# Optimization experiments

Measured on AMD Instinct MI355X. Metric: run time of the kernel, lower is better.

Reference implementation:

```python
import jax, jax.numpy as jnp
import numpy as np

B, N, K = 8, 2048, 16   # batch, points, neighbors (after dropping self)
EPS = 1e-5


def _bn(y, g, b, m, v):
    # eval-mode batchnorm over channel dim 1, y: [B,C,...]
    sh = (1, -1) + (1,) * (y.ndim - 2)
    inv = g.reshape(sh) / jnp.sqrt(v.reshape(sh) + EPS)
    return (y - m.reshape(sh)) * inv + b.reshape(sh)


def setup_inputs() -> dict:
    key = jax.random.key(0)
    ks = jax.random.split(key, 16)
    d = {}
    d["x"] = jax.random.normal(ks[0], (B, 3, N), dtype=jnp.float32)
    # pre: Conv1d(3->24, k=1) + BN
    d["w_pre"] = jax.random.normal(ks[1], (24, 3), dtype=jnp.float32) * 0.3
    d["b_pre"] = jax.random.normal(ks[2], (24,), dtype=jnp.float32) * 0.1
    d["g_pre"] = 1.0 + 0.1 * jax.random.normal(ks[3], (24,), dtype=jnp.float32)
    d["be_pre"] = 0.1 * jax.random.normal(ks[4], (24,), dtype=jnp.float32)
    d["m_pre"] = 0.1 * jax.random.normal(ks[5], (24,), dtype=jnp.float32)
    d["v_pre"] = jax.random.uniform(ks[6], (24,), minval=0.5, maxval=1.5, dtype=jnp.float32)
    # shared_mlp_1: Conv2d(48->12, 1, bias=False) + BN
    d["w1"] = jax.random.normal(ks[7], (12, 48), dtype=jnp.float32) * 0.15
    d["g1"] = 1.0 + 0.1 * jax.random.normal(ks[8], (12,), dtype=jnp.float32)
    d["be1"] = 0.1 * jax.random.normal(ks[9], (12,), dtype=jnp.float32)
    d["m1"] = 0.1 * jax.random.normal(ks[10], (12,), dtype=jnp.float32)
    d["v1"] = jax.random.uniform(ks[11], (12,), minval=0.5, maxval=1.5, dtype=jnp.float32)
    # shared_mlp_2: Conv2d(60->12, 1, bias=False) + BN
    d["w2"] = jax.random.normal(ks[12], (12, 60), dtype=jnp.float32) * 0.15
    d["g2"] = 1.0 + 0.1 * jax.random.normal(ks[13], (12,), dtype=jnp.float32)
    d["be2"] = 0.1 * jax.random.normal(ks[14], (12,), dtype=jnp.float32)
    d["m2"] = 0.1 * jax.random.normal(ks[15], (12,), dtype=jnp.float32)
    d["v2"] = jnp.ones((12,), dtype=jnp.float32)
    # shared_mlp_3: Conv2d(72->12, 1, bias=False), no BN
    d["w3"] = jax.random.normal(jax.random.fold_in(key, 99), (12, 72), dtype=jnp.float32) * 0.15
    return d


def reference(x, w_pre, b_pre, g_pre, be_pre, m_pre, v_pre,
              w1, g1, be1, m1, v1, w2, g2, be2, m2, v2, w3):
    # pre: 1x1 conv1d + BN + ReLU -> [B,24,N]
    pre = jnp.einsum('oc,bcn->bon', w_pre, x) + b_pre[None, :, None]
    pre = jax.nn.relu(_bn(pre, g_pre, be_pre, m_pre, v_pre))

    # kNN on xyz = x.detach(): [B,N,3]
    pts = jax.lax.stop_gradient(jnp.swapaxes(x, 1, 2))
    sq = jnp.sum(pts * pts, axis=-1)                              # [B,N]
    d2 = sq[:, :, None] + sq[:, None, :] - 2.0 * jnp.einsum('bnc,bmc->bnm', pts, pts)
    _, idx = jax.lax.top_k(-d2, K + 1)                             # nearest K+1 incl. self
    idx = idx[..., 1:]                                             # drop self -> [B,N,K]

    # gather neighbor features: [B,24,N,K]
    grouped = jax.vmap(lambda f, i: f[:, i])(pre, idx)
    center = jnp.broadcast_to(pre[..., None], grouped.shape)
    y = jnp.concatenate([center, grouped], axis=1)                 # [B,48,N,K]

    h1 = jax.nn.relu(_bn(jnp.einsum('oc,bcnk->bonk', w1, y), g1, be1, m1, v1))
    y = jnp.concatenate([h1, y], axis=1)                           # [B,60,N,K]
    h2 = jax.nn.relu(_bn(jnp.einsum('oc,bcnk->bonk', w2, y), g2, be2, m2, v2))
    y = jnp.concatenate([h2, y], axis=1)                           # [B,72,N,K]
    h3 = jnp.einsum('oc,bcnk->bonk', w3, y)
    y = jnp.concatenate([h3, y], axis=1)                           # [B,84,N,K]

    y = jnp.max(y, axis=-1)                                        # maxpool over neighbors -> [B,84,N]
    return jnp.concatenate([y, x], axis=1)                         # [B,87,N]
```

## Files before the change

### kernel.cpp

```cpp
#include <hip/hip_runtime.h>
#include <math.h>

#define EPS 1e-5f
#define NBATCH 8
#define NPTS 2048
#define KNB 16
#define BIG 3.2e38f

#define CHUNK_PTS 32
#define KNN_BLKS (NBATCH * 64)
#define THREADS 512
#define FUSED_LDS 49152

#define WS_PRE 0
#define WS_AUX (16384 * 24)
#define WS_IDX (WS_AUX + 16384 * 72)

__device__ __forceinline__ float dist2f(float mex, float mey, float mez,
                                        float sqn, float4 q) {
  float dot2 = fmaf(mex, q.x, fmaf(mey, q.y, __fmul_rn(mez, q.z)));
  return __fsub_rn(__fadd_rn(sqn, q.w), dot2);
}

template <bool HASSELF>
__device__ __forceinline__ void scan_slice(const float4* __restrict__ Cs, int selfc,
                                           float mex, float mey, float mez,
                                           float sqn, float L[16]) {
  for (int c0 = 0; c0 < 128; c0 += 16) {
    float S[16];
#pragma unroll
    for (int cc = 0; cc < 16; ++cc) {
      float4 q = Cs[c0 + cc];
      float d2 = dist2f(mex, mey, mez, sqn, q);
      if (HASSELF) S[cc] = ((c0 + cc) == selfc) ? BIG : d2;
      else         S[cc] = d2;
    }
#pragma unroll
    for (int pw = 1; pw < 16; pw <<= 1) {
#pragma unroll
      for (int k = pw; k >= 1; k >>= 1) {
#pragma unroll
        for (int j = (k & (pw - 1)); j + k < 16; j += 2 * k) {
#pragma unroll
          for (int i = 0; i < k; ++i) {
            int a = i + j, bq = i + j + k;
            if (bq < 16 && (a / (2 * pw) == bq / (2 * pw))) {
              float lo = fminf(S[a], S[bq]);
              float hi = fmaxf(S[a], S[bq]);
              S[a] = lo; S[bq] = hi;
            }
          }
        }
      }
    }
    float m[16];
#pragma unroll
    for (int i = 0; i < 16; ++i) m[i] = fminf(L[i], S[15 - i]);
#pragma unroll
    for (int d = 8; d >= 1; d >>= 1) {
#pragma unroll
      for (int i = 0; i < 16; ++i) {
        if (!(i & d)) {
          float lo = fminf(m[i], m[i | d]);
          float hi = fmaxf(m[i], m[i | d]);
          m[i] = lo; m[i | d] = hi;
        }
      }
    }
#pragma unroll
    for (int i = 0; i < 16; ++i) L[i] = m[i];
  }
}

__global__ __launch_bounds__(THREADS, 6) void fused_kernel(
    const float* __restrict__ x,
    const float* __restrict__ w_pre, const float* __restrict__ b_pre,
    const float* __restrict__ g_pre, const float* __restrict__ be_pre,
    const float* __restrict__ m_pre, const float* __restrict__ v_pre,
    const float* __restrict__ w1, const float* __restrict__ g1,
    const float* __restrict__ be1, const float* __restrict__ m1,
    const float* __restrict__ v1,
    const float* __restrict__ w2, const float* __restrict__ g2,
    const float* __restrict__ be2, const float* __restrict__ m2,
    const float* __restrict__ v2, const float* __restrict__ w3,
    float* __restrict__ pre, float* __restrict__ aux,
    int* __restrict__ knn_out) {
  extern __shared__ char smem[];
  float4* C4   = (float4*)smem;
  float* slist = (float*)(smem + 32768);
  float* fwp   = slist;
  float* fbp   = fwp + 72;
  float* fw1t  = fbp + 24;
  float* fb1   = fw1t + 576;
  float* fw2t  = fb1 + 12;
  float* fb2   = fw2t + 720;
  float* fw3t  = fb2 + 12;
  float* sinv1 = fw3t + 576;
  float* sinv2 = sinv1 + 12;
  float* sinvP = sinv2 + 12;
  float* sd2  = slist;
  int*   sidx = (int*)(slist + 640);
  int*   scnt = (int*)(slist + 1280);

  int tid = threadIdx.x;
  int bi = blockIdx.x;
  int b = bi >> 6, chunk = bi & 63;
  const float* xb = x + (size_t)b * 3 * NPTS;

  for (int j = tid; j < NPTS; j += THREADS) {
    float xx = xb[j], yy = xb[NPTS + j], zz = xb[2 * NPTS + j];
    float sq = __fadd_rn(__fadd_rn(__fmul_rn(xx, xx), __fmul_rn(yy, yy)),
                         __fmul_rn(zz, zz));
    C4[j] = make_float4(2.0f * xx, 2.0f * yy, 2.0f * zz, sq);
  }
  if (tid < 24) sinvP[tid] = g_pre[tid] / sqrtf(v_pre[tid] + EPS);
  if (tid < 12) { sinv1[tid] = g1[tid] / sqrtf(v1[tid] + EPS);
                  sinv2[tid] = g2[tid] / sqrtf(v2[tid] + EPS); }
  __syncthreads();
  if (tid < 72) fwp[tid] = w_pre[tid] * sinvP[tid / 3];
  if (tid < 24) fbp[tid] = (b_pre[tid] - m_pre[tid]) * sinvP[tid] + be_pre[tid];
  if (tid < 12) { fb1[tid] = be1[tid] - m1[tid] * sinv1[tid];
                  fb2[tid] = be2[tid] - m2[tid] * sinv2[tid]; }
  for (int j = tid; j < 576; j += THREADS) { int i = j / 12, o = j - i * 12; fw1t[j] = w1[o * 48 + i] * sinv1[o]; }
  for (int j = tid; j < 720; j += THREADS) { int i = j / 12, o = j - i * 12; fw2t[j] = w2[o * 60 + i] * sinv2[o]; }
  for (int j = tid; j < 576; j += THREADS) { int i = j / 12, o = j - i * 12; fw3t[j] = w3[o * 72 + 24 + i]; }
  __syncthreads();

  {
    int r = tid & 15, pt = tid >> 4;
    int n0 = chunk * CHUNK_PTS + pt;
    size_t pgl = (size_t)(b << 11) + n0;
    float x0 = xb[n0], x1 = xb[NPTS + n0], x2 = xb[2 * NPTS + n0];
    float pr[24];
#pragma unroll
    for (int c = 0; c < 24; ++c) {
      float v = fmaf(fwp[c * 3 + 0], x0,
                fmaf(fwp[c * 3 + 1], x1,
                fmaf(fwp[c * 3 + 2], x2, fbp[c])));
      pr[c] = fmaxf(v, 0.f);
    }
    if (r == 12) {
      float4* o4 = (float4*)(pre + pgl * 24);
#pragma unroll
      for (int i = 0; i < 6; ++i)
        o4[i] = make_float4(pr[4*i], pr[4*i+1], pr[4*i+2], pr[4*i+3]);
    }
    if (r < 12) {
      int o = r;
      float u1 = fb1[o], a1 = 0.f, u2 = fb2[o], a2 = 0.f, u3 = 0.f, a3 = 0.f;
#pragma unroll
      for (int i = 0; i < 24; ++i) {
        u1 = fmaf(fw1t[i * 12 + o],        pr[i], u1);
        a1 = fmaf(fw1t[(24 + i) * 12 + o], pr[i], a1);
        u2 = fmaf(fw2t[(12 + i) * 12 + o], pr[i], u2);
        a2 = fmaf(fw2t[(36 + i) * 12 + o], pr[i], a2);
        u3 = fmaf(fw3t[i * 12 + o],        pr[i], u3);
        a3 = fmaf(fw3t[(24 + i) * 12 + o], pr[i], a3);
      }
      float* A = aux + pgl * 72;
      A[o] = u1; A[12 + o] = u2; A[24 + o] = u3;
      A[36 + o] = a1; A[48 + o] = a2; A[60 + o] = a3;
    }
  }
  __syncthreads();

  int p = tid & 31, s = tid >> 5;
  int w = tid >> 6;
  int n = chunk * CHUNK_PTS + p;
  float4 me4 = C4[n];
  float mex = 0.5f * me4.x, mey = 0.5f * me4.y, mez = 0.5f * me4.z;
  float sqn = me4.w;
  const float4* Cs = C4 + s * 128;
  int selfc = n - s * 128;
  int wself = chunk >> 3;
  float L[16];
#pragma unroll
  for (int t = 0; t < 16; ++t) L[t] = BIG;
  if (w == wself) scan_slice<true >(Cs, selfc, mex, mey, mez, sqn, L);
  else            scan_slice<false>(Cs, selfc, mex, mey, mez, sqn, L);
  {
    float bb[16], m16[16];
#pragma unroll
    for (int i = 0; i < 16; ++i) bb[i] = __shfl_xor(L[i], 32, 64);
#pragma unroll
    for (int i = 0; i < 16; ++i) m16[i] = fminf(L[i], bb[15 - i]);
#pragma unroll
    for (int d = 8; d >= 1; d >>= 1) {
#pragma unroll
      for (int i = 0; i < 16; ++i) {
        if (!(i & d)) {
          float lo = fminf(m16[i], m16[i | d]);
          float hi = fmaxf(m16[i], m16[i | d]);
          m16[i] = lo; m16[i | d] = hi;
        }
      }
    }
    if (!(s & 1)) {
#pragma unroll
      for (int i = 0; i < 16; ++i) slist[(w * 16 + i) * 32 + p] = m16[i];
    }
  }
  __syncthreads();
  for (int W = 4; W >= 1; W >>= 1) {
    int u = tid >> 5;
    bool act = (u < W);
    float a[16], bb[16];
    if (act) {
#pragma unroll
      for (int i = 0; i < 16; ++i) a[i]  = slist[((2 * u) * 16 + i) * 32 + p];
#pragma unroll
      for (int i = 0; i < 16; ++i) bb[i] = slist[((2 * u + 1) * 16 + i) * 32 + p];
    }
    __syncthreads();
    if (act) {
      float m16[16];
#pragma unroll
      for (int i = 0; i < 16; ++i) m16[i] = fminf(a[i], bb[15 - i]);
#pragma unroll
      for (int d = 8; d >= 1; d >>= 1) {
#pragma unroll
        for (int i = 0; i < 16; ++i) {
          if (!(i & d)) {
            float lo = fminf(m16[i], m16[i | d]);
            float hi = fmaxf(m16[i], m16[i | d]);
            m16[i] = lo; m16[i | d] = hi;
          }
        }
      }
#pragma unroll
      for (int i = 0; i < 16; ++i) slist[(u * 16 + i) * 32 + p] = m16[i];
    }
    __syncthreads();
  }
  float tau = slist[15 * 32 + p];
  __syncthreads();
  for (int j = tid; j < 32 * 20; j += THREADS) sidx[j] = 0;
  if (tid < 32) scnt[tid] = 0;
  __syncthreads();
  if (w == wself) {
#pragma unroll 4
    for (int c = 0; c < 128; ++c) {
      float4 q = Cs[c];
      float d2 = dist2f(mex, mey, mez, sqn, q);
      int j = s * 128 + c;
      if (d2 <= tau && j != n) {
        int pos = atomicAdd(&scnt[p], 1);
        if (pos < 20) { sd2[p * 20 + pos] = d2; sidx[p * 20 + pos] = j; }
      }
    }
  } else {
#pragma unroll 4
    for (int c = 0; c < 128; ++c) {
      float4 q = Cs[c];
      float d2 = dist2f(mex, mey, mez, sqn, q);
      int j = s * 128 + c;
      if (d2 <= tau) {
        int pos = atomicAdd(&scnt[p], 1);
        if (pos < 20) { sd2[p * 20 + pos] = d2; sidx[p * 20 + pos] = j; }
      }
    }
  }
  __syncthreads();
  if (tid < 32) {
    int c = scnt[tid]; if (c > 20) c = 20;
    if (c > 16) {
      for (int t = 0; t < 16; ++t) {
        int best = t;
        for (int u = t + 1; u < c; ++u) {
          float da = sd2[tid * 20 + u], db = sd2[tid * 20 + best];
          int ia = sidx[tid * 20 + u], ib = sidx[tid * 20 + best];
          if (da < db || (da == db && ia < ib)) best = u;
        }
        float td = sd2[tid * 20 + t]; sd2[tid * 20 + t] = sd2[tid * 20 + best]; sd2[tid * 20 + best] = td;
        int ti = sidx[tid * 20 + t]; sidx[tid * 20 + t] = sidx[tid * 20 + best]; sidx[tid * 20 + best] = ti;
      }
    }
  }
  __syncthreads();
  {
    int pp = tid >> 4, kk = tid & 15;
    knn_out[((size_t)b * NPTS + chunk * CHUNK_PTS + pp) * KNB + kk] = sidx[pp * 20 + kk];
  }
}

__global__ __launch_bounds__(256) void mlp_kernel(
    const float* __restrict__ pre, const float* __restrict__ aux,
    const int* __restrict__ knn, const float* __restrict__ x,
    const float* __restrict__ w2, const float* __restrict__ g2,
    const float* __restrict__ v2, const float* __restrict__ w3,
    float* __restrict__ out) {
  __shared__ float sW2h[144], sW3h2[144], sW3h1[144];
  __shared__ float sout[87 * 16];
  int tid = threadIdx.x;
  if (tid < 144) {
    int o = tid / 12, i = tid - o * 12;
    float inv2 = g2[o] / sqrtf(v2[o] + EPS);
    sW2h[tid]  = w2[o * 60 + i] * inv2;
    sW3h2[tid] = w3[o * 72 + i];
    sW3h1[tid] = w3[o * 72 + 12 + i];
  }
  __syncthreads();
  int k = tid & 15, pl = tid >> 4;
  int p = blockIdx.x * 16 + pl;
  int b = p >> 11, n = p & (NPTS - 1);
  int nb = knn[(size_t)p * KNB + k];
  const float4* u4 = (const float4*)(aux + (size_t)p * 72);
  const float4* a4 = (const float4*)(aux + ((size_t)(b << 11) + nb) * 72 + 36);
  float uc[36], av[36];
#pragma unroll
  for (int i = 0; i < 9; ++i) {
    float4 t = u4[i];
    uc[4*i] = t.x; uc[4*i+1] = t.y; uc[4*i+2] = t.z; uc[4*i+3] = t.w;
    float4 t2 = a4[i];
    av[4*i] = t2.x; av[4*i+1] = t2.y; av[4*i+2] = t2.z; av[4*i+3] = t2.w;
  }
  float h1[12], h2[12], h3[12];
#pragma unroll
  for (int o = 0; o < 12; ++o) h1[o] = fmaxf(uc[o] + av[o], 0.f);
#pragma unroll
  for (int o = 0; o < 12; ++o) {
    float a = uc[12 + o] + av[12 + o];
#pragma unroll
    for (int i = 0; i < 12; ++i) a = fmaf(sW2h[o * 12 + i], h1[i], a);
    h2[o] = fmaxf(a, 0.f);
  }
#pragma unroll
  for (int o = 0; o < 12; ++o) {
    float a = uc[24 + o] + av[24 + o];
#pragma unroll
    for (int i = 0; i < 12; ++i) a = fmaf(sW3h2[o * 12 + i], h2[i], a);
#pragma unroll
    for (int i = 0; i < 12; ++i) a = fmaf(sW3h1[o * 12 + i], h1[i], a);
    h3[o] = a;
  }
  float nbf[24];
  const float4* pn4 = (const float4*)(pre + ((size_t)(b << 11) + nb) * 24);
#pragma unroll
  for (int i = 0; i < 6; ++i) {
    float4 t = pn4[i];
    nbf[4*i] = t.x; nbf[4*i+1] = t.y; nbf[4*i+2] = t.z; nbf[4*i+3] = t.w;
  }
#pragma unroll
  for (int m = 1; m < 16; m <<= 1) {
#pragma unroll
    for (int o = 0; o < 12; ++o) {
      h1[o] = fmaxf(h1[o], __shfl_xor(h1[o], m, 16));
      h2[o] = fmaxf(h2[o], __shfl_xor(h2[o], m, 16));
      h3[o] = fmaxf(h3[o], __shfl_xor(h3[o], m, 16));
    }
#pragma unroll
    for (int i = 0; i < 24; ++i)
      nbf[i] = fmaxf(nbf[i], __shfl_xor(nbf[i], m, 16));
  }
  if (k == 0) {
    const float4* c4 = (const float4*)(pre + (size_t)p * 24);
#pragma unroll
    for (int o = 0; o < 12; ++o) {
      sout[(0  + o) * 16 + pl] = h3[o];
      sout[(12 + o) * 16 + pl] = h2[o];
      sout[(24 + o) * 16 + pl] = h1[o];
    }
#pragma unroll
    for (int i = 0; i < 6; ++i) {
      float4 t = c4[i];
      sout[(36 + 4*i    ) * 16 + pl] = t.x;
      sout[(36 + 4*i + 1) * 16 + pl] = t.y;
      sout[(36 + 4*i + 2) * 16 + pl] = t.z;
      sout[(36 + 4*i + 3) * 16 + pl] = t.w;
    }
#pragma unroll
    for (int i = 0; i < 24; ++i) sout[(60 + i) * 16 + pl] = nbf[i];
    const float* xb = x + (size_t)b * 3 * NPTS + n;
    sout[84 * 16 + pl] = xb[0];
    sout[85 * 16 + pl] = xb[NPTS];
    sout[86 * 16 + pl] = xb[2 * NPTS];
  }
  __syncthreads();
  int n0 = (blockIdx.x * 16) & (NPTS - 1);
  float* ob = out + (size_t)b * 87 * NPTS;
  for (int j2 = tid; j2 < 87 * 16; j2 += 256) {
    int c = j2 >> 4, i = j2 & 15;
    ob[(size_t)c * NPTS + n0 + i] = sout[j2];
  }
}

extern "C" void kernel_launch(void* const* d_in, const int* in_sizes, int n_in,
                              void* d_out, int out_size, void* d_ws, size_t ws_size,
                              hipStream_t stream) {
  (void)in_sizes; (void)n_in; (void)out_size; (void)ws_size;
  const float* x     = (const float*)d_in[0];
  const float* w_pre = (const float*)d_in[1];
  const float* b_pre = (const float*)d_in[2];
  const float* g_pre = (const float*)d_in[3];
  const float* be_pre= (const float*)d_in[4];
  const float* m_pre = (const float*)d_in[5];
  const float* v_pre = (const float*)d_in[6];
  const float* w1    = (const float*)d_in[7];
  const float* g1    = (const float*)d_in[8];
  const float* be1   = (const float*)d_in[9];
  const float* m1    = (const float*)d_in[10];
  const float* v1    = (const float*)d_in[11];
  const float* w2    = (const float*)d_in[12];
  const float* g2    = (const float*)d_in[13];
  const float* be2   = (const float*)d_in[14];
  const float* m2    = (const float*)d_in[15];
  const float* v2    = (const float*)d_in[16];
  const float* w3    = (const float*)d_in[17];
  float* ws  = (float*)d_ws;
  float* pre = ws + WS_PRE;
  float* aux = ws + WS_AUX;
  int*   knn = (int*)(ws + WS_IDX);
  float* out = (float*)d_out;

  fused_kernel<<<KNN_BLKS, THREADS, FUSED_LDS, stream>>>(
      x, w_pre, b_pre, g_pre, be_pre, m_pre, v_pre,
      w1, g1, be1, m1, v1, w2, g2, be2, m2, v2, w3,
      pre, aux, knn);
  mlp_kernel<<<NBATCH * NPTS / 16, 256, 0, stream>>>(pre, aux, knn, x,
                                                     w2, g2, v2, w3, out);
}
```

Before: 151.5 us.

## Precompute point coordinate table in separate kernel and fold distance into FMAs

Adds a prep kernel that builds a per-batch float4 table of negated doubled coordinates and squared norms once in global memory, so each fused block copies it into LDS instead of recomputing it from strided x reads. The distance formula is rewritten as a single FMA chain using the negated coordinates, which saves an instruction per candidate. The second candidate-collection pass now reads coordinates from the global table (likely L2-cached) instead of LDS. The extra kernel launch and the global reads in that pass add cost, and the fused FMA can change rounding, which may alter neighbor ties.

```diff
diff --git a/kernel.cpp b/kernel.cpp
--- a/kernel.cpp
+++ b/kernel.cpp
@@ -15,11 +15,11 @@
 #define WS_PRE 0
 #define WS_AUX (16384 * 24)
 #define WS_IDX (WS_AUX + 16384 * 72)
+#define WS_C4G (WS_IDX + 16384 * 16)
 
 __device__ __forceinline__ float dist2f(float mex, float mey, float mez,
                                         float sqn, float4 q) {
-  float dot2 = fmaf(mex, q.x, fmaf(mey, q.y, __fmul_rn(mez, q.z)));
-  return __fsub_rn(__fadd_rn(sqn, q.w), dot2);
+  return fmaf(mex, q.x, fmaf(mey, q.y, fmaf(mez, q.z, __fadd_rn(sqn, q.w))));
 }
 
 template <bool HASSELF>
@@ -70,6 +70,17 @@
 #pragma unroll
     for (int i = 0; i < 16; ++i) L[i] = m[i];
   }
+}
+
+__global__ __launch_bounds__(256) void prep_kernel(
+    const float* __restrict__ x, float4* __restrict__ c4g) {
+  int i = blockIdx.x * 256 + threadIdx.x;
+  int b = i >> 11, n = i & (NPTS - 1);
+  const float* xb = x + (size_t)b * 3 * NPTS;
+  float xx = xb[n], yy = xb[NPTS + n], zz = xb[2 * NPTS + n];
+  float sq = __fadd_rn(__fadd_rn(__fmul_rn(xx, xx), __fmul_rn(yy, yy)),
+                       __fmul_rn(zz, zz));
+  c4g[i] = make_float4(-2.0f * xx, -2.0f * yy, -2.0f * zz, sq);
 }
 
 __global__ __launch_bounds__(THREADS, 6) void fused_kernel(
@@ -83,6 +94,7 @@
     const float* __restrict__ w2, const float* __restrict__ g2,
     const float* __restrict__ be2, const float* __restrict__ m2,
     const float* __restrict__ v2, const float* __restrict__ w3,
+    const float4* __restrict__ c4g,
     float* __restrict__ pre, float* __restrict__ aux,
     int* __restrict__ knn_out) {
   extern __shared__ char smem[];
@@ -105,14 +117,10 @@
   int tid = threadIdx.x;
   int bi = blockIdx.x;
   int b = bi >> 6, chunk = bi & 63;
+  int bq = b << 11;
   const float* xb = x + (size_t)b * 3 * NPTS;
 
-  for (int j = tid; j < NPTS; j += THREADS) {
-    float xx = xb[j], yy = xb[NPTS + j], zz = xb[2 * NPTS + j];
-    float sq = __fadd_rn(__fadd_rn(__fmul_rn(xx, xx), __fmul_rn(yy, yy)),
-                         __fmul_rn(zz, zz));
-    C4[j] = make_float4(2.0f * xx, 2.0f * yy, 2.0f * zz, sq);
-  }
+  for (int j = tid; j < NPTS; j += THREADS) C4[j] = c4g[bq + j];
   if (tid < 24) sinvP[tid] = g_pre[tid] / sqrtf(v_pre[tid] + EPS);
   if (tid < 12) { sinv1[tid] = g1[tid] / sqrtf(v1[tid] + EPS);
                   sinv2[tid] = g2[tid] / sqrtf(v2[tid] + EPS); }
@@ -129,7 +137,7 @@
   {
     int r = tid & 15, pt = tid >> 4;
     int n0 = chunk * CHUNK_PTS + pt;
-    size_t pgl = (size_t)(b << 11) + n0;
+    size_t pgl = (size_t)bq + n0;
     float x0 = xb[n0], x1 = xb[NPTS + n0], x2 = xb[2 * NPTS + n0];
     float pr[24];
 #pragma unroll
@@ -168,7 +176,7 @@
   int w = tid >> 6;
   int n = chunk * CHUNK_PTS + p;
   float4 me4 = C4[n];
-  float mex = 0.5f * me4.x, mey = 0.5f * me4.y, mez = 0.5f * me4.z;
+  float mex = -0.5f * me4.x, mey = -0.5f * me4.y, mez = -0.5f * me4.z;
   float sqn = me4.w;
   const float4* Cs = C4 + s * 128;
   int selfc = n - s * 128;
@@ -237,26 +245,29 @@
   for (int j = tid; j < 32 * 20; j += THREADS) sidx[j] = 0;
   if (tid < 32) scnt[tid] = 0;
   __syncthreads();
-  if (w == wself) {
+  {
+    const float4* Cg = c4g + bq + s * 128;
+    if (w == wself) {
 #pragma unroll 4
-    for (int c = 0; c < 128; ++c) {
-      float4 q = Cs[c];
-      float d2 = dist2f(mex, mey, mez, sqn, q);
-      int j = s * 128 + c;
-      if (d2 <= tau && j != n) {
-        int pos = atomicAdd(&scnt[p], 1);
-        if (pos < 20) { sd2[p * 20 + pos] = d2; sidx[p * 20 + pos] = j; }
-      }
-    }
-  } else {
+      for (int c = 0; c < 128; ++c) {
+        float4 q = Cg[c];
+        float d2 = dist2f(mex, mey, mez, sqn, q);
+        int j = s * 128 + c;
+        if (d2 <= tau && j != n) {
+          int pos = atomicAdd(&scnt[p], 1);
+          if (pos < 20) { sd2[p * 20 + pos] = d2; sidx[p * 20 + pos] = j; }
+        }
+      }
+    } else {
 #pragma unroll 4
-    for (int c = 0; c < 128; ++c) {
-      float4 q = Cs[c];
-      float d2 = dist2f(mex, mey, mez, sqn, q);
-      int j = s * 128 + c;
-      if (d2 <= tau) {
-        int pos = atomicAdd(&scnt[p], 1);
-        if (pos < 20) { sd2[p * 20 + pos] = d2; sidx[p * 20 + pos] = j; }
+      for (int c = 0; c < 128; ++c) {
+        float4 q = Cg[c];
+        float d2 = dist2f(mex, mey, mez, sqn, q);
+        int j = s * 128 + c;
+        if (d2 <= tau) {
+          int pos = atomicAdd(&scnt[p], 1);
+          if (pos < 20) { sd2[p * 20 + pos] = d2; sidx[p * 20 + pos] = j; }
+        }
       }
     }
   }
@@ -410,12 +421,14 @@
   float* pre = ws + WS_PRE;
   float* aux = ws + WS_AUX;
   int*   knn = (int*)(ws + WS_IDX);
+  float4* c4g = (float4*)(ws + WS_C4G);
   float* out = (float*)d_out;
 
+  prep_kernel<<<NBATCH * NPTS / 256, 256, 0, stream>>>(x, c4g);
   fused_kernel<<<KNN_BLKS, THREADS, FUSED_LDS, stream>>>(
       x, w_pre, b_pre, g_pre, be_pre, m_pre, v_pre,
       w1, g1, be1, m1, v1, w2, g2, be2, m2, v2, w3,
-      pre, aux, knn);
+      c4g, pre, aux, knn);
   mlp_kernel<<<NBATCH * NPTS / 16, 256, 0, stream>>>(pre, aux, knn, x,
                                                      w2, g2, v2, w3, out);
 }
```

New measurement: 160.3 us. 1.06x slower.

## Software-pipeline KNN distance batches and move candidate buffers to separate LDS

Applied to the files above, without the earlier changes.

Restructures the KNN slice scan into a fully unrolled, double-buffered sequence: the next 16 distances are loaded and computed while the previous batch is sorted and merged, aiming to hide LDS latency behind the sorting network. The candidate buffers (sd2/sidx/scnt) get their own LDS region so they can be zeroed at kernel start, which removes two barriers before the refinement pass. The distance calculation folds the -2 factor into the stored coordinates so it becomes one fma chain with no separate subtraction. In exchange, LDS per block and register pressure rise, and launch_bounds min-blocks is lowered from 6 to 4, which may reduce occupancy and changes float rounding of the distances slightly.

```diff
diff --git a/kernel.cpp b/kernel.cpp
--- a/kernel.cpp
+++ b/kernel.cpp
@@ -10,7 +10,7 @@
 #define CHUNK_PTS 32
 #define KNN_BLKS (NBATCH * 64)
 #define THREADS 512
-#define FUSED_LDS 49152
+#define FUSED_LDS 54400
 
 #define WS_PRE 0
 #define WS_AUX (16384 * 24)
@@ -18,61 +18,90 @@
 
 __device__ __forceinline__ float dist2f(float mex, float mey, float mez,
                                         float sqn, float4 q) {
-  float dot2 = fmaf(mex, q.x, fmaf(mey, q.y, __fmul_rn(mez, q.z)));
-  return __fsub_rn(__fadd_rn(sqn, q.w), dot2);
+  return fmaf(mex, q.x, fmaf(mey, q.y, fmaf(mez, q.z, __fadd_rn(sqn, q.w))));
+}
+
+__device__ __forceinline__ void sort16(float S[16]) {
+#pragma unroll
+  for (int pw = 1; pw < 16; pw <<= 1) {
+#pragma unroll
+    for (int k = pw; k >= 1; k >>= 1) {
+#pragma unroll
+      for (int j = (k & (pw - 1)); j + k < 16; j += 2 * k) {
+#pragma unroll
+        for (int i = 0; i < k; ++i) {
+          int a = i + j, bq = i + j + k;
+          if (bq < 16 && (a / (2 * pw) == bq / (2 * pw))) {
+            float lo = fminf(S[a], S[bq]);
+            float hi = fmaxf(S[a], S[bq]);
+            S[a] = lo; S[bq] = hi;
+          }
+        }
+      }
+    }
+  }
+}
+
+__device__ __forceinline__ void clean16(float m[16]) {
+#pragma unroll
+  for (int d = 8; d >= 1; d >>= 1) {
+#pragma unroll
+    for (int i = 0; i < 16; ++i) {
+      if (!(i & d)) {
+        float lo = fminf(m[i], m[i | d]);
+        float hi = fmaxf(m[i], m[i | d]);
+        m[i] = lo; m[i | d] = hi;
+      }
+    }
+  }
+}
+
+__device__ __forceinline__ void merge16(float L[16], const float S[16]) {
+  float m[16];
+#pragma unroll
+  for (int i = 0; i < 16; ++i) m[i] = fminf(L[i], S[15 - i]);
+  clean16(m);
+#pragma unroll
+  for (int i = 0; i < 16; ++i) L[i] = m[i];
+}
+
+template <bool HASSELF>
+__device__ __forceinline__ void dist_batch(const float4* __restrict__ Cs, int c0,
+                                           int selfc, float mex, float mey,
+                                           float mez, float sqn, float S[16]) {
+#pragma unroll
+  for (int cc = 0; cc < 16; ++cc) {
+    float4 q = Cs[c0 + cc];
+    float d2 = dist2f(mex, mey, mez, sqn, q);
+    if (HASSELF) S[cc] = ((c0 + cc) == selfc) ? BIG : d2;
+    else         S[cc] = d2;
+  }
 }
 
 template <bool HASSELF>
 __device__ __forceinline__ void scan_slice(const float4* __restrict__ Cs, int selfc,
                                            float mex, float mey, float mez,
                                            float sqn, float L[16]) {
-  for (int c0 = 0; c0 < 128; c0 += 16) {
-    float S[16];
-#pragma unroll
-    for (int cc = 0; cc < 16; ++cc) {
-      float4 q = Cs[c0 + cc];
-      float d2 = dist2f(mex, mey, mez, sqn, q);
-      if (HASSELF) S[cc] = ((c0 + cc) == selfc) ? BIG : d2;
-      else         S[cc] = d2;
-    }
-#pragma unroll
-    for (int pw = 1; pw < 16; pw <<= 1) {
-#pragma unroll
-      for (int k = pw; k >= 1; k >>= 1) {
-#pragma unroll
-        for (int j = (k & (pw - 1)); j + k < 16; j += 2 * k) {
-#pragma unroll
-          for (int i = 0; i < k; ++i) {
-            int a = i + j, bq = i + j + k;
-            if (bq < 16 && (a / (2 * pw) == bq / (2 * pw))) {
-              float lo = fminf(S[a], S[bq]);
-              float hi = fmaxf(S[a], S[bq]);
-              S[a] = lo; S[bq] = hi;
-            }
-          }
-        }
-      }
-    }
-    float m[16];
-#pragma unroll
-    for (int i = 0; i < 16; ++i) m[i] = fminf(L[i], S[15 - i]);
-#pragma unroll
-    for (int d = 8; d >= 1; d >>= 1) {
-#pragma unroll
-      for (int i = 0; i < 16; ++i) {
-        if (!(i & d)) {
-          float lo = fminf(m[i], m[i | d]);
-          float hi = fmaxf(m[i], m[i | d]);
-          m[i] = lo; m[i | d] = hi;
-        }
-      }
-    }
-#pragma unroll
-    for (int i = 0; i < 16; ++i) L[i] = m[i];
-  }
-}
-
-__global__ __launch_bounds__(THREADS, 6) void fused_kernel(
+  float Sa[16], Sb[16];
+  dist_batch<HASSELF>(Cs,   0, selfc, mex, mey, mez, sqn, Sa);
+  dist_batch<HASSELF>(Cs,  16, selfc, mex, mey, mez, sqn, Sb);
+  sort16(Sa); merge16(L, Sa);
+  dist_batch<HASSELF>(Cs,  32, selfc, mex, mey, mez, sqn, Sa);
+  sort16(Sb); merge16(L, Sb);
+  dist_batch<HASSELF>(Cs,  48, selfc, mex, mey, mez, sqn, Sb);
+  sort16(Sa); merge16(L, Sa);
+  dist_batch<HASSELF>(Cs,  64, selfc, mex, mey, mez, sqn, Sa);
+  sort16(Sb); merge16(L, Sb);
+  dist_batch<HASSELF>(Cs,  80, selfc, mex, mey, mez, sqn, Sb);
+  sort16(Sa); merge16(L, Sa);
+  dist_batch<HASSELF>(Cs,  96, selfc, mex, mey, mez, sqn, Sa);
+  sort16(Sb); merge16(L, Sb);
+  dist_batch<HASSELF>(Cs, 112, selfc, mex, mey, mez, sqn, Sb);
+  sort16(Sa); merge16(L, Sa);
+  sort16(Sb); merge16(L, Sb);
+}
+
+__global__ __launch_bounds__(THREADS, 4) void fused_kernel(
     const float* __restrict__ x,
     const float* __restrict__ w_pre, const float* __restrict__ b_pre,
     const float* __restrict__ g_pre, const float* __restrict__ be_pre,
@@ -98,9 +127,9 @@
   float* sinv1 = fw3t + 576;
   float* sinv2 = sinv1 + 12;
   float* sinvP = sinv2 + 12;
-  float* sd2  = slist;
-  int*   sidx = (int*)(slist + 640);
-  int*   scnt = (int*)(slist + 1280);
+  float* sd2  = (float*)(smem + 49152);
+  int*   sidx = (int*)(smem + 51712);
+  int*   scnt = (int*)(smem + 54272);
 
   int tid = threadIdx.x;
   int bi = blockIdx.x;
@@ -111,8 +140,10 @@
     float xx = xb[j], yy = xb[NPTS + j], zz = xb[2 * NPTS + j];
     float sq = __fadd_rn(__fadd_rn(__fmul_rn(xx, xx), __fmul_rn(yy, yy)),
                          __fmul_rn(zz, zz));
-    C4[j] = make_float4(2.0f * xx, 2.0f * yy, 2.0f * zz, sq);
-  }
+    C4[j] = make_float4(-2.0f * xx, -2.0f * yy, -2.0f * zz, sq);
+  }
+  for (int j = tid; j < 32 * 20; j += THREADS) sidx[j] = 0;
+  if (tid < 32) scnt[tid] = 0;
   if (tid < 24) sinvP[tid] = g_pre[tid] / sqrtf(v_pre[tid] + EPS);
   if (tid < 12) { sinv1[tid] = g1[tid] / sqrtf(v1[tid] + EPS);
                   sinv2[tid] = g2[tid] / sqrtf(v2[tid] + EPS); }
@@ -168,7 +199,7 @@
   int w = tid >> 6;
   int n = chunk * CHUNK_PTS + p;
   float4 me4 = C4[n];
-  float mex = 0.5f * me4.x, mey = 0.5f * me4.y, mez = 0.5f * me4.z;
+  float mex = -0.5f * me4.x, mey = -0.5f * me4.y, mez = -0.5f * me4.z;
   float sqn = me4.w;
   const float4* Cs = C4 + s * 128;
   int selfc = n - s * 128;
@@ -184,17 +215,7 @@
     for (int i = 0; i < 16; ++i) bb[i] = __shfl_xor(L[i], 32, 64);
 #pragma unroll
     for (int i = 0; i < 16; ++i) m16[i] = fminf(L[i], bb[15 - i]);
-#pragma unroll
-    for (int d = 8; d >= 1; d >>= 1) {
-#pragma unroll
-      for (int i = 0; i < 16; ++i) {
-        if (!(i & d)) {
-          float lo = fminf(m16[i], m16[i | d]);
-          float hi = fmaxf(m16[i], m16[i | d]);
-          m16[i] = lo; m16[i | d] = hi;
-        }
-      }
-    }
+    clean16(m16);
     if (!(s & 1)) {
 #pragma unroll
       for (int i = 0; i < 16; ++i) slist[(w * 16 + i) * 32 + p] = m16[i];
@@ -216,27 +237,13 @@
       float m16[16];
 #pragma unroll
       for (int i = 0; i < 16; ++i) m16[i] = fminf(a[i], bb[15 - i]);
-#pragma unroll
-      for (int d = 8; d >= 1; d >>= 1) {
-#pragma unroll
-        for (int i = 0; i < 16; ++i) {
-          if (!(i & d)) {
-            float lo = fminf(m16[i], m16[i | d]);
-            float hi = fmaxf(m16[i], m16[i | d]);
-            m16[i] = lo; m16[i | d] = hi;
-          }
-        }
-      }
+      clean16(m16);
 #pragma unroll
       for (int i = 0; i < 16; ++i) slist[(u * 16 + i) * 32 + p] = m16[i];
     }
     __syncthreads();
   }
   float tau = slist[15 * 32 + p];
-  __syncthreads();
-  for (int j = tid; j < 32 * 20; j += THREADS) sidx[j] = 0;
-  if (tid < 32) scnt[tid] = 0;
-  __syncthreads();
   if (w == wself) {
 #pragma unroll 4
     for (int c = 0; c < 128; ++c) {
```

Measured after the change: 153.2 us. No clear change (+1.1%).
